# Kernel optimization log

Measured on AMD Instinct MI355X. Metric: run time of the kernel, lower is better.

The kernel has to match this reference:

```python
import jax, jax.numpy as jnp
import numpy as np

H = 16           # num_heads
D = 1024         # num_units
QD = KD = VD = 64
LN_EPS = 1e-5


def _xavier(key, shape):
    fan_in, fan_out = shape[-2], shape[-1]
    std = np.sqrt(2.0 / (fan_in + fan_out))
    return jax.random.normal(key, shape, dtype=jnp.float32) * std


def setup_inputs() -> dict:
    key = jax.random.key(0)
    ks = jax.random.split(key, 10)
    B, Sq, Sk = 8, 1024, 1024
    return {
        "query": jax.random.normal(ks[0], (B, Sq, D), dtype=jnp.float32),
        "keys": jax.random.normal(ks[1], (B, Sk, D), dtype=jnp.float32),
        "values": jax.random.normal(ks[2], (B, Sk, D), dtype=jnp.float32),
        "Wq": _xavier(ks[3], (H, D, QD)),
        "Wk": _xavier(ks[4], (H, D, KD)),
        "Wv": _xavier(ks[5], (H, D, VD)),
        "Wp": _xavier(ks[6], (H * VD, D)),   # proj, stored input-major: y = x @ Wp + bp
        "bp": jnp.zeros((D,), dtype=jnp.float32),
        "gamma": jnp.ones((D,), dtype=jnp.float32),
        "beta": jnp.zeros((D,), dtype=jnp.float32),
    }


def reference(query, keys, values, Wq, Wk, Wv, Wp, bp, gamma, beta):
    B, Sq, _ = query.shape
    Sk = keys.shape[1]
    # RepeatLinear per head: [B,S,D] x [H,D,e] -> [H,B,S,e]
    Q = jnp.einsum("bsd,hde->hbse", query, Wq)
    K = jnp.einsum("bsd,hde->hbse", keys, Wk)
    V = jnp.einsum("bsd,hde->hbse", values, Wv)
    # NOTE: original scales by sqrt(num_units), not sqrt(key_dim)
    temper = jnp.asarray(np.sqrt(D), dtype=Q.dtype)
    scores = jnp.einsum("hbqe,hbke->hbqk", Q, K) / temper  # [H,B,Sq,Sk]
    attn = jax.nn.softmax(scores, axis=-1)
    # dropout is identity in eval mode
    out = jnp.einsum("hbqk,hbke->hbqe", attn, V)           # [H,B,Sq,VD]
    # torch.cat(torch.split(out, B, 0), -1): head-major feature concat
    out = out.transpose(1, 2, 0, 3).reshape(B, Sq, H * VD)
    out = out @ Wp + bp                                     # proj
    # residual + LayerNorm
    y = out + query
    mu = jnp.mean(y, axis=-1, keepdims=True)
    var = jnp.var(y, axis=-1, keepdims=True)
    y = (y - mu) / jnp.sqrt(var + LN_EPS) * gamma + beta
    return y, attn.reshape(H * B, Sq, Sk)
```

## Files before the change

### kernel.cpp

```cpp
#include <hip/hip_runtime.h>
#include <hip/hip_bf16.h>

#define H_ 16
#define B_ 8
#define S_ 1024
#define D_ 1024
#define E_ 64
#define HB_ 128
#define LN_EPS 1e-5f
#define LOG2E 1.4426950408889634f

typedef unsigned short u16;
typedef __bf16 bf16x8 __attribute__((ext_vector_type(8)));
typedef u16 u16x8 __attribute__((ext_vector_type(8)));
typedef u16 u16x4 __attribute__((ext_vector_type(4)));
typedef float f32x4 __attribute__((ext_vector_type(4)));
typedef unsigned u32x2 __attribute__((ext_vector_type(2)));

#define MFMA16(a, b, c) __builtin_amdgcn_mfma_f32_16x16x32_bf16( \
    __builtin_bit_cast(bf16x8, (a)), __builtin_bit_cast(bf16x8, (b)), (c), 0, 0, 0)

#define GLL16(gp, lp) __builtin_amdgcn_global_load_lds( \
    (const __attribute__((address_space(1))) void*)(gp), \
    (__attribute__((address_space(3))) void*)(lp), 16, 0, 0)

__device__ __forceinline__ unsigned cvt_pk_bf16(float lo, float hi) {
  unsigned r;
  asm("v_cvt_pk_bf16_f32 %0, %1, %2" : "=v"(r) : "v"(lo), "v"(hi));
  return r;
}
__device__ __forceinline__ u16x4 pk4(f32x4 v) {
  union { unsigned u[2]; u16x4 s; } r;
  r.u[0] = cvt_pk_bf16(v[0], v[1]);
  r.u[1] = cvt_pk_bf16(v[2], v[3]);
  return r.s;
}
__device__ __forceinline__ float exp2_hw(float x) {
  float r;
  asm("v_exp_f32 %0, %1" : "=v"(r) : "v"(x));
  return r;
}
__device__ __forceinline__ float bfhi(unsigned u) {
  return __builtin_bit_cast(float, u & 0xFFFF0000u);
}
__device__ __forceinline__ float bflo(unsigned u) {
  return __builtin_bit_cast(float, u << 16);
}

__global__ __launch_bounds__(256) void k_prep(
    const float* __restrict__ Wq, const float* __restrict__ Wk,
    const float* __restrict__ Wv, const float* __restrict__ Wp,
    u16* __restrict__ Wt,
    const float* __restrict__ Xq, const float* __restrict__ Xk,
    const float* __restrict__ Xv, u16* __restrict__ Xdst) {
  const int bid = blockIdx.x;
  if (bid >= 1024) {
    const int b2 = bid - 1024;
    const int t = b2 >> 12;
    const float* X = t == 0 ? Xq : t == 1 ? Xk : Xv;
    u16* Y = Xdst + (size_t)t * (8 << 20);
    int i = ((b2 & 4095) * 256 + threadIdx.x) * 8;
    f32x4 a = *(const f32x4*)(X + i);
    f32x4 b = *(const f32x4*)(X + i + 4);
    union { unsigned u[4]; u16x8 s; } v;
    v.u[0] = cvt_pk_bf16(a[0], a[1]);
    v.u[1] = cvt_pk_bf16(a[2], a[3]);
    v.u[2] = cvt_pk_bf16(b[0], b[1]);
    v.u[3] = cvt_pk_bf16(b[2], b[3]);
    *(u16x8*)(Y + i) = v.s;
    return;
  }
  __shared__ float tile[64][65];
  const int which = bid >> 8, r = bid & 255;
  const float* src;
  int R, C, rt, ct;
  float scale = 1.0f;
  size_t soff, doff;
  if (which < 3) {
    src = which == 0 ? Wq : which == 1 ? Wk : Wv;
    if (which == 0) scale = LOG2E / 32.0f;
    int slice = r & 15, rtile = r >> 4;
    R = 1024; C = 64; rt = rtile * 64; ct = 0;
    soff = (size_t)slice * 65536;
    doff = (size_t)which * (1 << 20) + (size_t)slice * 65536;
  } else {
    src = Wp;
    R = 1024; C = 1024; rt = (r & 15) * 64; ct = (r >> 4) * 64;
    soff = 0; doff = (size_t)3 * (1 << 20);
  }
  const float* I = src + soff;
  u16* O = Wt + doff;
  const int t = threadIdx.x;
  const int c4 = (t & 15) * 4;
  #pragma unroll
  for (int i = 0; i < 4; i++) {
    int rr = i * 16 + (t >> 4);
    f32x4 v = *(const f32x4*)&I[(size_t)(rt + rr) * C + ct + c4];
    tile[rr][c4 + 0] = v[0]; tile[rr][c4 + 1] = v[1];
    tile[rr][c4 + 2] = v[2]; tile[rr][c4 + 3] = v[3];
  }
  __syncthreads();
  #pragma unroll
  for (int i = 0; i < 4; i++) {
    int oc = i * 16 + (t >> 4);
    f32x4 tv;
    #pragma unroll
    for (int rr = 0; rr < 4; rr++) tv[rr] = tile[c4 + rr][oc] * scale;
    *(u16x4*)&O[(size_t)(ct + oc) * R + rt + c4] = pk4(tv);
  }
}

#define STAGE_TILES() do { \
    GLL16(Ag + kt,             AsB0); \
    GLL16(Ag + 64 * 1024 + kt, AsB0 + 2048); \
    GLL16(Bg + kt,             BsB0); \
    GLL16(Bg + 64 * 1024 + kt, BsB0 + 2048); \
  } while (0)

#define READ_FRAGS() do { \
    _Pragma("unroll") \
    for (int mi = 0; mi < 4; mi++) \
      af[mi] = *(const u16x8*)&As[(wr * 64 + mi * 16 + lr) * 32 + lg * 8]; \
    _Pragma("unroll") \
    for (int ni = 0; ni < 4; ni++) \
      bf[ni] = *(const u16x8*)&Bs[(wc * 64 + ni * 16 + lr) * 32 + lg * 8]; \
  } while (0)

template<int MODE>
__global__ __launch_bounds__(256) void k_gemm(
    const u16* __restrict__ X0, const u16* __restrict__ Ball,
    u16* __restrict__ O0, u16* __restrict__ O1, u16* __restrict__ O2,
    float* __restrict__ Pf, const float* __restrict__ bp,
    const float* __restrict__ query) {
  const int bid = blockIdx.x + (blockIdx.y << 6);
  const int bx  = ((bid & 7) << 3) + ((bid >> 3) & 7);
  const int by  = bid >> 6;
  const int l  = threadIdx.x & 63;
  const int w  = threadIdx.x >> 6;
  const int lr = l & 15, lg = l >> 4;
  const int wr = w >> 1, wc = w & 1;
  const int m0 = bx * 128, n0 = by * 128;

  const u16* A = (MODE == 0) ? X0 + (size_t)(by >> 3) * (8 << 20) : X0;

  __shared__ __align__(16) u16 As[128 * 32];
  __shared__ __align__(16) u16 Bs[128 * 32];

  const int srow = w * 16 + (l >> 2);
  const int scol = (l & 3) * 8;
  const u16* Ag = A    + (size_t)(m0 + srow) * 1024 + scol;
  const u16* Bg = Ball + (size_t)(n0 + srow) * 1024 + scol;
  u16* AsB0 = As + w * 512;
  u16* BsB0 = Bs + w * 512;

  f32x4 acc[4][4] = {};
  u16x8 af[4], bf[4];

  if (MODE == 2 || by < 16) {
    for (int kt = 0; kt < 1024; kt += 32) {
      STAGE_TILES();
      __syncthreads();
      READ_FRAGS();
      #pragma unroll
      for (int mi = 0; mi < 4; mi++)
        #pragma unroll
        for (int ni = 0; ni < 4; ni++)
          acc[mi][ni] = MFMA16(bf[ni], af[mi], acc[mi][ni]);
      __syncthreads();
    }
  } else {
    for (int kt = 0; kt < 1024; kt += 32) {
      STAGE_TILES();
      __syncthreads();
      READ_FRAGS();
      #pragma unroll
      for (int mi = 0; mi < 4; mi++)
        #pragma unroll
        for (int ni = 0; ni < 4; ni++)
          acc[mi][ni] = MFMA16(af[mi], bf[ni], acc[mi][ni]);
      __syncthreads();
    }
  }

  if (MODE == 0 && by < 16) {
    u16* Out = (by >= 8) ? O1 : O0;
    const int h = (by & 7) * 2 + wc;
    #pragma unroll
    for (int mi = 0; mi < 4; mi++) {
      int s = m0 + wr * 64 + mi * 16 + lr;
      int bb = s >> 10, ss = s & 1023;
      #pragma unroll
      for (int ni = 0; ni < 4; ni++)
        *(u16x4*)&Out[((size_t)(h * 8 + bb) * 1024 + ss) * 64 + ni * 16 + lg * 4] =
            pk4(acc[mi][ni]);
    }
  } else if (MODE == 0) {
    const int byv = by - 16;
    const int h = byv * 2 + wc;
    #pragma unroll
    for (int mi = 0; mi < 4; mi++) {
      int s = m0 + wr * 64 + mi * 16 + lg * 4;
      int bb = s >> 10, ss = s & 1023;
      #pragma unroll
      for (int ni = 0; ni < 4; ni++)
        *(u16x4*)&O2[((size_t)(h * 8 + bb) * 64 + ni * 16 + lr) * 1024 + ss] =
            pk4(acc[mi][ni]);
    }
  } else {
    #pragma unroll
    for (int mi = 0; mi < 4; mi++) {
      int m = m0 + wr * 64 + mi * 16 + lr;
      #pragma unroll
      for (int ni = 0; ni < 4; ni++) {
        int n = n0 + wc * 64 + ni * 16 + lg * 4;
        f32x4 b4 = *(const f32x4*)(bp + n);
        f32x4 q4 = *(const f32x4*)(query + (size_t)m * 1024 + n);
        f32x4 o = acc[mi][ni] + b4 + q4;
        *(f32x4*)(Pf + (size_t)m * 1024 + n) = o;
      }
    }
  }
}

__global__ __launch_bounds__(256, 4) void k_attn(const u16* __restrict__ Qb,
    const u16* __restrict__ Kb, const u16* __restrict__ Vtb,
    float* __restrict__ attn_out, u16* __restrict__ AO) {
  const int bid = blockIdx.x;
  const int xcd = bid & 7, within = bid >> 3;
  const int qt = within & 63;
  const int hb = xcd * 16 + (within >> 6);
  const int w  = threadIdx.x >> 6;
  const int l  = threadIdx.x & 63;
  const int lr = l & 15, lg = l >> 4;
  const int q0 = qt * 16;

  __shared__ __align__(16) u16 pbuf[16 * 1024];
  __shared__ float wmaxs[4][16];
  __shared__ float wsums[4][16];

  const u16* Qp = Qb + ((size_t)hb * 1024 + q0 + lr) * 64 + lg * 8;
  const u16* Kp = Kb + ((size_t)hb * 1024 + w * 256 + lr) * 64 + lg * 8;
  u16x8 q_lo = *(const u16x8*)Qp;
  u16x8 q_hi = *(const u16x8*)(Qp + 32);

  f32x4 sacc[16] = {};
  __builtin_amdgcn_s_setprio(1);
  #pragma unroll
  for (int j = 0; j < 16; j++) {
    u16x8 k0 = *(const u16x8*)(Kp + (size_t)j * 16 * 64);
    u16x8 k1 = *(const u16x8*)(Kp + (size_t)j * 16 * 64 + 32);
    sacc[j] = MFMA16(k0, q_lo, sacc[j]);
    sacc[j] = MFMA16(k1, q_hi, sacc[j]);
  }
  __builtin_amdgcn_s_setprio(0);

  float mx = sacc[0][0];
  #pragma unroll
  for (int j = 0; j < 16; j++)
    #pragma unroll
    for (int r = 0; r < 4; r++) mx = fmaxf(mx, sacc[j][r]);
  mx = fmaxf(mx, __shfl_xor(mx, 16));
  mx = fmaxf(mx, __shfl_xor(mx, 32));

  float sum = 0.f;
  #pragma unroll
  for (int j = 0; j < 16; j++)
    #pragma unroll
    for (int r = 0; r < 4; r++) {
      float p = exp2_hw(sacc[j][r] - mx);
      sacc[j][r] = p;
      sum += p;
    }
  sum += __shfl_xor(sum, 16);
  sum += __shfl_xor(sum, 32);

  const u16* Vp = Vtb + ((size_t)hb * 64 + w * 16 + lr) * 1024 + lg * 8;
  u16x8 vp0 = *(const u16x8*)(Vp + 0);
  u16x8 vp1 = *(const u16x8*)(Vp + 32);
  u16x8 vp2 = *(const u16x8*)(Vp + 64);
  u16x8 vp3 = *(const u16x8*)(Vp + 96);

  #pragma unroll
  for (int j = 0; j < 16; j++) {
    int k0 = w * 256 + j * 16 + lg * 4;
    int byte = (lr * 2048 + k0 * 2) ^ ((lr & 7) << 4);
    *(u16x4*)((char*)pbuf + byte) = pk4(sacc[j]);
  }
  if (l < 16) { wmaxs[w][lr] = mx; wsums[w][lr] = sum; }

  __syncthreads();

  #pragma unroll
  for (int rr = 0; rr < 4; rr++) {
    const int row = w * 4 + rr;
    float M0 = wmaxs[0][row], M1 = wmaxs[1][row], M2 = wmaxs[2][row], M3 = wmaxs[3][row];
    float GM = fmaxf(fmaxf(M0, M1), fmaxf(M2, M3));
    float E0 = exp2_hw(M0 - GM), E1 = exp2_hw(M1 - GM);
    float E2 = exp2_hw(M2 - GM), E3 = exp2_hw(M3 - GM);
    float IV = 1.0f / (wsums[0][row] * E0 + wsums[1][row] * E1 +
                       wsums[2][row] * E2 + wsums[3][row] * E3);
    float cs0 = E0 * IV, cs1 = E1 * IV, cs2 = E2 * IV, cs3 = E3 * IV;
    float* Ap = attn_out + ((size_t)hb * 1024 + q0 + row) * 1024;
    #pragma unroll
    for (int c = 0; c < 4; c++) {
      float sc = c == 0 ? cs0 : c == 1 ? cs1 : c == 2 ? cs2 : cs3;
      int byte = (row * 2048 + (c * 256 + l * 4) * 2) ^ ((row & 7) << 4);
      u32x2 d = *(u32x2*)((char*)pbuf + byte);
      f32x4 v;
      v[0] = bflo(d[0]) * sc;
      v[1] = bfhi(d[0]) * sc;
      v[2] = bflo(d[1]) * sc;
      v[3] = bfhi(d[1]) * sc;
      __builtin_nontemporal_store(v, (f32x4*)(Ap + c * 256 + l * 4));
    }
  }

  float m0v = wmaxs[0][lr], m1v = wmaxs[1][lr], m2v = wmaxs[2][lr], m3v = wmaxs[3][lr];
  float gmax = fmaxf(fmaxf(m0v, m1v), fmaxf(m2v, m3v));
  float e0 = exp2_hw(m0v - gmax), e1 = exp2_hw(m1v - gmax);
  float e2 = exp2_hw(m2v - gmax), e3 = exp2_hw(m3v - gmax);
  float gsum = wsums[0][lr] * e0 + wsums[1][lr] * e1 + wsums[2][lr] * e2 + wsums[3][lr] * e3;
  float inv = 1.0f / gsum;
  float c0 = e0 * inv, c1 = e1 * inv, c2 = e2 * inv, c3 = e3 * inv;

  f32x4 o0 = {}, o1 = {}, o2 = {}, o3 = {};
  __builtin_amdgcn_s_setprio(1);
  #pragma unroll
  for (int i = 0; i < 4; i++)
    #pragma unroll
    for (int kk = 0; kk < 8; kk++) {
      int kb = i * 256 + kk * 32 + lg * 8;
      int byte = (lr * 2048 + kb * 2) ^ ((lr & 7) << 4);
      u16x8 p = *(u16x8*)((char*)pbuf + byte);
      u16x8 v;
      if (i == 0 && kk == 0) v = vp0;
      else if (i == 0 && kk == 1) v = vp1;
      else if (i == 0 && kk == 2) v = vp2;
      else if (i == 0 && kk == 3) v = vp3;
      else v = *(const u16x8*)(Vp + i * 256 + kk * 32);
      if (i == 0) o0 = MFMA16(v, p, o0);
      else if (i == 1) o1 = MFMA16(v, p, o1);
      else if (i == 2) o2 = MFMA16(v, p, o2);
      else o3 = MFMA16(v, p, o3);
    }
  __builtin_amdgcn_s_setprio(0);

  const int bb = hb & 7, hh = hb >> 3;
  f32x4 oc;
  #pragma unroll
  for (int r = 0; r < 4; r++)
    oc[r] = o0[r] * c0 + o1[r] * c1 + o2[r] * c2 + o3[r] * c3;
  *(u16x4*)&AO[((size_t)bb * 1024 + q0 + lr) * 1024 + hh * 64 + w * 16 + lg * 4] = pk4(oc);
}

__global__ __launch_bounds__(256) void k_ln(const float* __restrict__ P,
    const float* __restrict__ gamma, const float* __restrict__ beta,
    float* __restrict__ y) {
  const int row = blockIdx.x * 4 + (threadIdx.x >> 6);
  const int l = threadIdx.x & 63;
  const float* p = P + (size_t)row * 1024 + l * 4;
  f32x4 v[4];
  float s = 0.f, s2 = 0.f;
  #pragma unroll
  for (int i = 0; i < 4; i++) {
    v[i] = *(const f32x4*)(p + i * 256);
    #pragma unroll
    for (int r = 0; r < 4; r++) { s += v[i][r]; s2 += v[i][r] * v[i][r]; }
  }
  #pragma unroll
  for (int off = 1; off < 64; off <<= 1) {
    s += __shfl_xor(s, off);
    s2 += __shfl_xor(s2, off);
  }
  float mu = s * (1.0f / 1024.0f);
  float var = s2 * (1.0f / 1024.0f) - mu * mu;
  float rstd = rsqrtf(var + LN_EPS);
  float* yp = y + (size_t)row * 1024 + l * 4;
  #pragma unroll
  for (int i = 0; i < 4; i++) {
    f32x4 g = *(const f32x4*)(gamma + l * 4 + i * 256);
    f32x4 b = *(const f32x4*)(beta + l * 4 + i * 256);
    f32x4 o;
    #pragma unroll
    for (int r = 0; r < 4; r++) o[r] = (v[i][r] - mu) * rstd * g[r] + b[r];
    __builtin_nontemporal_store(o, (f32x4*)(yp + i * 256));
  }
}

extern "C" void kernel_launch(void* const* d_in, const int* in_sizes, int n_in,
                              void* d_out, int out_size, void* d_ws, size_t ws_size,
                              hipStream_t stream) {
  const float* query  = (const float*)d_in[0];
  const float* keys   = (const float*)d_in[1];
  const float* values = (const float*)d_in[2];
  const float* Wq     = (const float*)d_in[3];
  const float* Wk     = (const float*)d_in[4];
  const float* Wv     = (const float*)d_in[5];
  const float* Wp     = (const float*)d_in[6];
  const float* bp     = (const float*)d_in[7];
  const float* gamma  = (const float*)d_in[8];
  const float* beta   = (const float*)d_in[9];

  float* y        = (float*)d_out;
  float* attn_out = (float*)d_out + (size_t)B_ * S_ * D_;

  u16* ws  = (u16*)d_ws;
  u16* Wqt = ws;
  u16* Wpt = Wqt + (3 << 20);
  u16* Xqb = Wqt + (4 << 20);
  u16* Qb  = Xqb + (24 << 20);
  u16* Kb  = Qb + (8 << 20);
  u16* Vtb = Kb + (8 << 20);
  u16* AO  = Vtb + (8 << 20);
  float* P = (float*)Xqb;

  k_prep<<<13312, 256, 0, stream>>>(Wq, Wk, Wv, Wp, Wqt, query, keys, values, Xqb);

  k_gemm<0><<<dim3(64, 24), 256, 0, stream>>>(Xqb, Wqt, Qb, Kb, Vtb, nullptr, nullptr, nullptr);

  k_attn<<<8192, 256, 0, stream>>>(Qb, Kb, Vtb, attn_out, AO);

  k_gemm<2><<<dim3(64, 8), 256, 0, stream>>>(AO, Wpt, nullptr, nullptr, nullptr, P, bp, query);
  k_ln<<<2048, 256, 0, stream>>>(P, gamma, beta, y);
}
```

Baseline: 388.8 us.

## Chain PV accumulation with online rescaling and prefetch V in register batches

```diff
diff --git a/kernel.cpp b/kernel.cpp
--- a/kernel.cpp
+++ b/kernel.cpp
@@ -290,6 +290,28 @@
 
   __syncthreads();
 
+  float m0v = wmaxs[0][lr], m1v = wmaxs[1][lr], m2v = wmaxs[2][lr], m3v = wmaxs[3][lr];
+  float gmax = fmaxf(fmaxf(m0v, m1v), fmaxf(m2v, m3v));
+  float gsum = wsums[0][lr] * exp2_hw(m0v - gmax) + wsums[1][lr] * exp2_hw(m1v - gmax)
+             + wsums[2][lr] * exp2_hw(m2v - gmax) + wsums[3][lr] * exp2_hw(m3v - gmax);
+  float r01 = exp2_hw(m0v - m1v);
+  float r12 = exp2_hw(m1v - m2v);
+  float r23 = exp2_hw(m2v - m3v);
+  float c3  = exp2_hw(m3v - gmax) / gsum;
+
+  u16x8 vp4 = *(const u16x8*)(Vp + 128);
+  u16x8 vp5 = *(const u16x8*)(Vp + 160);
+  u16x8 vp6 = *(const u16x8*)(Vp + 192);
+  u16x8 vp7 = *(const u16x8*)(Vp + 224);
+  u16x8 vq0 = *(const u16x8*)(Vp + 256);
+  u16x8 vq1 = *(const u16x8*)(Vp + 288);
+  u16x8 vq2 = *(const u16x8*)(Vp + 320);
+  u16x8 vq3 = *(const u16x8*)(Vp + 352);
+  u16x8 vq4 = *(const u16x8*)(Vp + 384);
+  u16x8 vq5 = *(const u16x8*)(Vp + 416);
+  u16x8 vq6 = *(const u16x8*)(Vp + 448);
+  u16x8 vq7 = *(const u16x8*)(Vp + 480);
+
   #pragma unroll
   for (int rr = 0; rr < 4; rr++) {
     const int row = w * 4 + rr;
@@ -315,41 +337,66 @@
     }
   }
 
-  float m0v = wmaxs[0][lr], m1v = wmaxs[1][lr], m2v = wmaxs[2][lr], m3v = wmaxs[3][lr];
-  float gmax = fmaxf(fmaxf(m0v, m1v), fmaxf(m2v, m3v));
-  float e0 = exp2_hw(m0v - gmax), e1 = exp2_hw(m1v - gmax);
-  float e2 = exp2_hw(m2v - gmax), e3 = exp2_hw(m3v - gmax);
-  float gsum = wsums[0][lr] * e0 + wsums[1][lr] * e1 + wsums[2][lr] * e2 + wsums[3][lr] * e3;
-  float inv = 1.0f / gsum;
-  float c0 = e0 * inv, c1 = e1 * inv, c2 = e2 * inv, c3 = e3 * inv;
-
-  f32x4 o0 = {}, o1 = {}, o2 = {}, o3 = {};
+  f32x4 o = {};
   __builtin_amdgcn_s_setprio(1);
-  #pragma unroll
-  for (int i = 0; i < 4; i++)
-    #pragma unroll
-    for (int kk = 0; kk < 8; kk++) {
-      int kb = i * 256 + kk * 32 + lg * 8;
-      int byte = (lr * 2048 + kb * 2) ^ ((lr & 7) << 4);
-      u16x8 p = *(u16x8*)((char*)pbuf + byte);
-      u16x8 v;
-      if (i == 0 && kk == 0) v = vp0;
-      else if (i == 0 && kk == 1) v = vp1;
-      else if (i == 0 && kk == 2) v = vp2;
-      else if (i == 0 && kk == 3) v = vp3;
-      else v = *(const u16x8*)(Vp + i * 256 + kk * 32);
-      if (i == 0) o0 = MFMA16(v, p, o0);
-      else if (i == 1) o1 = MFMA16(v, p, o1);
-      else if (i == 2) o2 = MFMA16(v, p, o2);
-      else o3 = MFMA16(v, p, o3);
-    }
+  #define PBUF_P(i, kk) (*(u16x8*)((char*)pbuf + \
+      ((lr * 2048 + ((i) * 256 + (kk) * 32 + lg * 8) * 2) ^ ((lr & 7) << 4))))
+  o = MFMA16(vp0, PBUF_P(0, 0), o);
+  o = MFMA16(vp1, PBUF_P(0, 1), o);
+  o = MFMA16(vp2, PBUF_P(0, 2), o);
+  o = MFMA16(vp3, PBUF_P(0, 3), o);
+  o = MFMA16(vp4, PBUF_P(0, 4), o);
+  o = MFMA16(vp5, PBUF_P(0, 5), o);
+  o = MFMA16(vp6, PBUF_P(0, 6), o);
+  o = MFMA16(vp7, PBUF_P(0, 7), o);
+  vp0 = *(const u16x8*)(Vp + 512);
+  vp1 = *(const u16x8*)(Vp + 544);
+  vp2 = *(const u16x8*)(Vp + 576);
+  vp3 = *(const u16x8*)(Vp + 608);
+  vp4 = *(const u16x8*)(Vp + 640);
+  vp5 = *(const u16x8*)(Vp + 672);
+  vp6 = *(const u16x8*)(Vp + 704);
+  vp7 = *(const u16x8*)(Vp + 736);
+  o *= r01;
+  o = MFMA16(vq0, PBUF_P(1, 0), o);
+  o = MFMA16(vq1, PBUF_P(1, 1), o);
+  o = MFMA16(vq2, PBUF_P(1, 2), o);
+  o = MFMA16(vq3, PBUF_P(1, 3), o);
+  o = MFMA16(vq4, PBUF_P(1, 4), o);
+  o = MFMA16(vq5, PBUF_P(1, 5), o);
+  o = MFMA16(vq6, PBUF_P(1, 6), o);
+  o = MFMA16(vq7, PBUF_P(1, 7), o);
+  vq0 = *(const u16x8*)(Vp + 768);
+  vq1 = *(const u16x8*)(Vp + 800);
+  vq2 = *(const u16x8*)(Vp + 832);
+  vq3 = *(const u16x8*)(Vp + 864);
+  vq4 = *(const u16x8*)(Vp + 896);
+  vq5 = *(const u16x8*)(Vp + 928);
+  vq6 = *(const u16x8*)(Vp + 960);
+  vq7 = *(const u16x8*)(Vp + 992);
+  o *= r12;
+  o = MFMA16(vp0, PBUF_P(2, 0), o);
+  o = MFMA16(vp1, PBUF_P(2, 1), o);
+  o = MFMA16(vp2, PBUF_P(2, 2), o);
+  o = MFMA16(vp3, PBUF_P(2, 3), o);
+  o = MFMA16(vp4, PBUF_P(2, 4), o);
+  o = MFMA16(vp5, PBUF_P(2, 5), o);
+  o = MFMA16(vp6, PBUF_P(2, 6), o);
+  o = MFMA16(vp7, PBUF_P(2, 7), o);
+  o *= r23;
+  o = MFMA16(vq0, PBUF_P(3, 0), o);
+  o = MFMA16(vq1, PBUF_P(3, 1), o);
+  o = MFMA16(vq2, PBUF_P(3, 2), o);
+  o = MFMA16(vq3, PBUF_P(3, 3), o);
+  o = MFMA16(vq4, PBUF_P(3, 4), o);
+  o = MFMA16(vq5, PBUF_P(3, 5), o);
+  o = MFMA16(vq6, PBUF_P(3, 6), o);
+  o = MFMA16(vq7, PBUF_P(3, 7), o);
   __builtin_amdgcn_s_setprio(0);
+  #undef PBUF_P
 
   const int bb = hb & 7, hh = hb >> 3;
-  f32x4 oc;
-  #pragma unroll
-  for (int r = 0; r < 4; r++)
-    oc[r] = o0[r] * c0 + o1[r] * c1 + o2[r] * c2 + o3[r] * c3;
+  f32x4 oc = o * c3;
   *(u16x4*)&AO[((size_t)bb * 1024 + q0 + lr) * 1024 + hh * 64 + w * 16 + lg * 4] = pk4(oc);
 }
 
```

Measured after the change: 388.0 us. Within noise of the previous version (-0.2%).
